# Optimization experiments

Measured on AMD Instinct MI355X. Metric: run time of the kernel, lower is better.

The kernel has to match this reference:

```python
import jax, jax.numpy as jnp
import numpy as np

N_RAYS = 65536   # 256x256 image
N_PTS = 128      # samples per ray
FEAT = 3         # RGB
FAR_DELTA = 1e10 # sentinel delta for last sample, as in the torch module


def setup_inputs() -> dict:
    key = jax.random.key(0)
    k1, k2, k3 = jax.random.split(key, 3)
    # depths along each ray must be increasing (deltas computed by diff)
    depth_values = jnp.sort(
        jax.random.uniform(k1, (N_RAYS, N_PTS), jnp.float32, 2.0, 6.0), axis=-1)
    density = jax.random.uniform(k2, (N_RAYS, N_PTS), jnp.float32)  # non-negative
    feature = jax.random.uniform(k3, (N_RAYS, N_PTS, FEAT), jnp.float32)
    return {"depth_values": depth_values, "density": density, "feature": feature}


def reference(depth_values, density, feature):
    n_rays, n_pts = depth_values.shape
    # deltas: consecutive depth differences, huge value appended for last bin
    deltas = jnp.concatenate(
        [depth_values[:, 1:] - depth_values[:, :-1],
         jnp.full((n_rays, 1), FAR_DELTA, depth_values.dtype)], axis=-1)
    tau = density * deltas                              # [n_rays, n_pts]
    # transmittance T_i = exp(-sum_{j<i} tau_j) (exclusive cumsum in log space)
    log_T = -jnp.concatenate(
        [jnp.zeros((n_rays, 1), tau.dtype), jnp.cumsum(tau[:, :-1], axis=-1)],
        axis=-1)
    weights = jnp.exp(log_T) * (1.0 - jnp.exp(-tau))    # [n_rays, n_pts]
    feat_out = jnp.einsum('np,npf->nf', weights, feature)         # [n_rays, F]
    depth_out = jnp.sum(weights * depth_values, axis=-1, keepdims=True)
    return jnp.concatenate([feat_out, depth_out], axis=-1)        # [n_rays, F+1]
```

## Files before the change

### kernel.cpp

```cpp
#include <hip/hip_runtime.h>

#define N_RAYS 65536
#define N_PTS 128
#define FEAT 3
#define FAR_DELTA 1e10f

#define NBLOCKS 2048
#define RAYS_PER_ITER 8
#define NITERS (N_RAYS / (NBLOCKS * RAYS_PER_ITER))

__global__ __launch_bounds__(256, 8) void volrend_kernel(
    const float* __restrict__ depth,
    const float* __restrict__ density,
    const float* __restrict__ feature,
    float* __restrict__ out)
{
    __shared__ float4 sfeat[RAYS_PER_ITER * (N_PTS * FEAT / 4)];

    const int tid  = threadIdx.x;
    const int sl   = tid & 31;
    const int rloc = tid >> 5;

    for (int it = 0; it < NITERS; ++it) {
        const int grp = (int)blockIdx.x + it * NBLOCKS;
        const int ray = grp * RAYS_PER_ITER + rloc;

        const float4 d   = *(const float4*)(depth   + ray * N_PTS + 4 * sl);
        const float4 rho = *(const float4*)(density + ray * N_PTS + 4 * sl);

        const float4* fsrc = (const float4*)feature
                           + (size_t)grp * (RAYS_PER_ITER * 96) + tid;
        float4 s0 = fsrc[0];
        float4 s1 = fsrc[256];
        float4 s2 = fsrc[512];

        if (it) __syncthreads();
        sfeat[tid]       = s0;
        sfeat[tid + 256] = s1;
        sfeat[tid + 512] = s2;
        __syncthreads();

        float nd = __shfl_down(d.x, 1);
        float t0 = rho.x * (d.y - d.x);
        float t1 = rho.y * (d.z - d.y);
        float t2 = rho.z * (d.w - d.z);
        float t3 = rho.w * ((sl == 31) ? FAR_DELTA : (nd - d.w));
        float p1 = t0, p2 = p1 + t1, p3 = p2 + t2, tot = p3 + t3;

        float e = __shfl_up(tot, 1);
        if (sl == 0) e = 0.0f;
        #pragma unroll
        for (int off = 1; off < 32; off <<= 1) {
            float u = __shfl_up(e, off);
            if (sl >= off) e += u;
        }

        float T0 = __expf(-e);
        float T1 = __expf(-(e + p1));
        float T2 = __expf(-(e + p2));
        float T3 = __expf(-(e + p3));
        float T4 = __expf(-(e + tot));
        float w0 = T0 - T1, w1 = T1 - T2, w2 = T2 - T3, w3 = T3 - T4;

        float acc3 = w0 * d.x + w1 * d.y + w2 * d.z + w3 * d.w;

        const float4* frow = &sfeat[rloc * 96 + sl * 3];
        float4 fa = frow[0], fb = frow[1], fc = frow[2];
        float acc0 = w0 * fa.x + w1 * fa.w + w2 * fb.z + w3 * fc.y;
        float acc1 = w0 * fa.y + w1 * fb.x + w2 * fb.w + w3 * fc.z;
        float acc2 = w0 * fa.z + w1 * fb.y + w2 * fc.x + w3 * fc.w;

        #pragma unroll
        for (int off = 16; off > 0; off >>= 1) {
            acc0 += __shfl_xor(acc0, off);
            acc1 += __shfl_xor(acc1, off);
            acc2 += __shfl_xor(acc2, off);
            acc3 += __shfl_xor(acc3, off);
        }
        if (sl == 0) {
            *(float4*)(out + ray * 4) = make_float4(acc0, acc1, acc2, acc3);
        }
    }
}

extern "C" void kernel_launch(void* const* d_in, const int* in_sizes, int n_in,
                              void* d_out, int out_size, void* d_ws, size_t ws_size,
                              hipStream_t stream) {
    const float* depth   = (const float*)d_in[0];
    const float* density = (const float*)d_in[1];
    const float* feature = (const float*)d_in[2];
    float* out = (float*)d_out;

    dim3 grid(NBLOCKS);
    dim3 block(256);
    volrend_kernel<<<grid, block, 0, stream>>>(depth, density, feature, out);
}
```

Before: 193.9 us.

## Drop LDS staging, load features directly per lane and prefetch next ray pair

```diff
diff --git a/kernel.cpp b/kernel.cpp
--- a/kernel.cpp
+++ b/kernel.cpp
@@ -1,51 +1,53 @@
 #include <hip/hip_runtime.h>
 
 #define N_RAYS 65536
-#define N_PTS 128
-#define FEAT 3
+#define N_PTS  128
 #define FAR_DELTA 1e10f
 
+#define BLOCK   256
 #define NBLOCKS 2048
-#define RAYS_PER_ITER 8
-#define NITERS (N_RAYS / (NBLOCKS * RAYS_PER_ITER))
+#define NWAVES  (NBLOCKS * (BLOCK / 64))
+#define NPAIRS  (N_RAYS / 2)
+#define NPASS   (NPAIRS / NWAVES)
 
-__global__ __launch_bounds__(256, 8) void volrend_kernel(
+__global__ __launch_bounds__(BLOCK, 6) void volrend_kernel(
     const float* __restrict__ depth,
     const float* __restrict__ density,
     const float* __restrict__ feature,
     float* __restrict__ out)
 {
-    __shared__ float4 sfeat[RAYS_PER_ITER * (N_PTS * FEAT / 4)];
+    const int lane = threadIdx.x & 63;
+    const int sl   = lane & 31;
+    const int g    = (int)blockIdx.x * (BLOCK / 64) + (threadIdx.x >> 6);
 
-    const int tid  = threadIdx.x;
-    const int sl   = tid & 31;
-    const int rloc = tid >> 5;
+    float4 d, rho, f0, f1, f2;
+    float4 pd, pr, pf0, pf1, pf2;
 
-    for (int it = 0; it < NITERS; ++it) {
-        const int grp = (int)blockIdx.x + it * NBLOCKS;
-        const int ray = grp * RAYS_PER_ITER + rloc;
+#define LOADP(p_, D_, R_, F0_, F1_, F2_)                                      \
+    do {                                                                      \
+        size_t rb_ = (size_t)(2 * (p_)) * N_PTS + 4 * lane;                   \
+        D_ = *(const float4*)(depth + rb_);                                   \
+        R_ = *(const float4*)(density + rb_);                                 \
+        const float* fp_ = feature + (size_t)(2 * (p_)) * (N_PTS * 3)         \
+                         + 12 * lane;                                         \
+        F0_ = *(const float4*)(fp_);                                          \
+        F1_ = *(const float4*)(fp_ + 4);                                      \
+        F2_ = *(const float4*)(fp_ + 8);                                      \
+    } while (0)
 
-        const float4 d   = *(const float4*)(depth   + ray * N_PTS + 4 * sl);
-        const float4 rho = *(const float4*)(density + ray * N_PTS + 4 * sl);
+    LOADP(g, d, rho, f0, f1, f2);
 
-        const float4* fsrc = (const float4*)feature
-                           + (size_t)grp * (RAYS_PER_ITER * 96) + tid;
-        float4 s0 = fsrc[0];
-        float4 s1 = fsrc[256];
-        float4 s2 = fsrc[512];
+#pragma unroll
+    for (int p = 0; p < NPASS; ++p) {
+        if (p + 1 < NPASS)
+            LOADP((p + 1) * NWAVES + g, pd, pr, pf0, pf1, pf2);
 
-        if (it) __syncthreads();
-        sfeat[tid]       = s0;
-        sfeat[tid + 256] = s1;
-        sfeat[tid + 512] = s2;
-        __syncthreads();
-
-        float nd = __shfl_down(d.x, 1);
+        float nx = __shfl_down(d.x, 1);
         float t0 = rho.x * (d.y - d.x);
         float t1 = rho.y * (d.z - d.y);
         float t2 = rho.z * (d.w - d.z);
-        float t3 = rho.w * ((sl == 31) ? FAR_DELTA : (nd - d.w));
-        float p1 = t0, p2 = p1 + t1, p3 = p2 + t2, tot = p3 + t3;
+        float t3 = rho.w * ((sl == 31) ? FAR_DELTA : (nx - d.w));
+        float q1 = t0, q2 = q1 + t1, q3 = q2 + t2, tot = q3 + t3;
 
         float e = __shfl_up(tot, 1);
         if (sl == 0) e = 0.0f;
@@ -56,31 +58,32 @@
         }
 
         float T0 = __expf(-e);
-        float T1 = __expf(-(e + p1));
-        float T2 = __expf(-(e + p2));
-        float T3 = __expf(-(e + p3));
+        float T1 = __expf(-(e + q1));
+        float T2 = __expf(-(e + q2));
+        float T3 = __expf(-(e + q3));
         float T4 = __expf(-(e + tot));
         float w0 = T0 - T1, w1 = T1 - T2, w2 = T2 - T3, w3 = T3 - T4;
 
-        float acc3 = w0 * d.x + w1 * d.y + w2 * d.z + w3 * d.w;
-
-        const float4* frow = &sfeat[rloc * 96 + sl * 3];
-        float4 fa = frow[0], fb = frow[1], fc = frow[2];
-        float acc0 = w0 * fa.x + w1 * fa.w + w2 * fb.z + w3 * fc.y;
-        float acc1 = w0 * fa.y + w1 * fb.x + w2 * fb.w + w3 * fc.z;
-        float acc2 = w0 * fa.z + w1 * fb.y + w2 * fc.x + w3 * fc.w;
+        float a3 = w0 * d.x  + w1 * d.y  + w2 * d.z  + w3 * d.w;
+        float a0 = w0 * f0.x + w1 * f0.w + w2 * f1.z + w3 * f2.y;
+        float a1 = w0 * f0.y + w1 * f1.x + w2 * f1.w + w3 * f2.z;
+        float a2 = w0 * f0.z + w1 * f1.y + w2 * f2.x + w3 * f2.w;
 
         #pragma unroll
         for (int off = 16; off > 0; off >>= 1) {
-            acc0 += __shfl_xor(acc0, off);
-            acc1 += __shfl_xor(acc1, off);
-            acc2 += __shfl_xor(acc2, off);
-            acc3 += __shfl_xor(acc3, off);
+            a0 += __shfl_xor(a0, off);
+            a1 += __shfl_xor(a1, off);
+            a2 += __shfl_xor(a2, off);
+            a3 += __shfl_xor(a3, off);
         }
         if (sl == 0) {
-            *(float4*)(out + ray * 4) = make_float4(acc0, acc1, acc2, acc3);
+            int ray = 2 * (p * NWAVES + g) + (lane >> 5);
+            *(float4*)(out + (size_t)ray * 4) = make_float4(a0, a1, a2, a3);
         }
+
+        d = pd; rho = pr; f0 = pf0; f1 = pf1; f2 = pf2;
     }
+#undef LOADP
 }
 
 extern "C" void kernel_launch(void* const* d_in, const int* in_sizes, int n_in,
@@ -92,6 +95,6 @@
     float* out = (float*)d_out;
 
     dim3 grid(NBLOCKS);
-    dim3 block(256);
+    dim3 block(BLOCK);
     volrend_kernel<<<grid, block, 0, stream>>>(depth, density, feature, out);
 }
```

Measured after the change: 194.6 us. About the same (+0.3%).
